# Optimization experiments

Hardware: AMD Instinct MI355X
Metric: run time of the kernel (lower is better)

The kernel has to match this reference:

```python
import jax, jax.numpy as jnp
import numpy as np

BN_EPS = 1e-5


def _gin_layer(x, src, dst, W, b, num_nodes):
    # GINConv with eps=0: h_i = MLP(x_i + sum_{j in N(i)} x_j)
    agg = jax.ops.segment_sum(x[src], dst, num_segments=num_nodes)  # [N, F]
    h = (x + agg) @ W + b
    return jax.nn.relu(h)


def _batchnorm(h, gamma, beta):
    # training-mode BatchNorm1d: biased batch stats over the node dim
    mean = jnp.mean(h, axis=0)
    var = jnp.mean(jnp.square(h - mean), axis=0)
    return (h - mean) * jax.lax.rsqrt(var + BN_EPS) * gamma + beta


def setup_inputs() -> dict:
    key = jax.random.key(0)
    N, E, F, H = 50000, 800000, 128, 128
    ks = jax.random.split(key, 6)
    x = jax.random.normal(ks[0], (N, F), dtype=jnp.float32)
    edge_index = jax.random.randint(ks[1], (2, E), 0, N, dtype=jnp.int64)
    W1 = jax.random.normal(ks[2], (F, H), dtype=jnp.float32) * 0.05
    b1 = jnp.zeros((H,), dtype=jnp.float32)
    W2 = jax.random.normal(ks[3], (H, H), dtype=jnp.float32) * 0.05
    b2 = jnp.zeros((H,), dtype=jnp.float32)
    g1 = jnp.ones((H,), dtype=jnp.float32)
    be1 = jnp.zeros((H,), dtype=jnp.float32)
    g2 = jnp.ones((H,), dtype=jnp.float32)
    be2 = jnp.zeros((H,), dtype=jnp.float32)
    return {"x": x, "edge_index": edge_index, "W1": W1, "b1": b1,
            "W2": W2, "b2": b2, "g1": g1, "be1": be1, "g2": g2, "be2": be2}


def reference(x, edge_index, W1, b1, W2, b2, g1, be1, g2, be2):
    N = x.shape[0]
    src, dst = edge_index[0], edge_index[1]
    h = _gin_layer(x, src, dst, W1, b1, N)
    h = _batchnorm(h, g1, be1)
    h = _gin_layer(h, src, dst, W2, b2, N)
    return _batchnorm(h, g2, be2)
```

## Files before the change

kernel.cpp:

```cpp
#include <hip/hip_runtime.h>
#include <hip/hip_fp16.h>

#define FDIM 128
#define NGRP 8

typedef _Float16 half8_t __attribute__((ext_vector_type(8)));
typedef _Float16 half4_t __attribute__((ext_vector_type(4)));
typedef float float4_t __attribute__((ext_vector_type(4)));


__global__ void zero_kernel(int* __restrict__ p, int n) {
  int i = blockIdx.x * blockDim.x + threadIdx.x;
  if (i < n) p[i] = 0;
}

__global__ void hist_part_kernel(const int* __restrict__ dst, int* __restrict__ deg,
                                 int E, int step) {
  int grp = blockIdx.x & (NGRP - 1);
  int nb = gridDim.x >> 3, bid = blockIdx.x >> 3;
  int lo = grp * step, hi = lo + step;
  int E4 = E >> 2;
  const int4* d4 = (const int4*)dst;
  for (int i = bid * blockDim.x + threadIdx.x; i < E4; i += nb * blockDim.x) {
    int4 d = d4[i];
    if (d.x >= lo && d.x < hi) atomicAdd(&deg[d.x], 1);
    if (d.y >= lo && d.y < hi) atomicAdd(&deg[d.y], 1);
    if (d.z >= lo && d.z < hi) atomicAdd(&deg[d.z], 1);
    if (d.w >= lo && d.w < hi) atomicAdd(&deg[d.w], 1);
  }
  for (int e = (E4 << 2) + bid * blockDim.x + threadIdx.x; e < E; e += nb * blockDim.x) {
    int d = dst[e];
    if (d >= lo && d < hi) atomicAdd(&deg[d], 1);
  }
}

__global__ void scan1_kernel(const int* __restrict__ deg, int* __restrict__ csums, int N) {
  __shared__ int sh[256];
  int t = threadIdx.x, b = blockIdx.x;
  int base = b * 1024;
  int s = 0;
#pragma unroll
  for (int i = 0; i < 4; i++) {
    int idx = base + t + 256 * i;
    if (idx < N) s += deg[idx];
  }
  sh[t] = s; __syncthreads();
  for (int off = 128; off > 0; off >>= 1) {
    if (t < off) sh[t] += sh[t + off];
    __syncthreads();
  }
  if (t == 0) csums[b] = sh[0];
}

__global__ void scan2_kernel(const int* __restrict__ csums, int* __restrict__ coffs, int nchunk) {
  __shared__ int sh[256];
  int t = threadIdx.x;
  int v = (t < nchunk) ? csums[t] : 0;
  sh[t] = v; __syncthreads();
  for (int off = 1; off < 256; off <<= 1) {
    int u = (t >= off) ? sh[t - off] : 0;
    __syncthreads();
    sh[t] += u;
    __syncthreads();
  }
  if (t < nchunk) coffs[t] = sh[t] - v;
}

__global__ void scan3_kernel(const int* __restrict__ deg, const int* __restrict__ coffs,
                             int* __restrict__ row_start, int* __restrict__ fill_pos, int N) {
  __shared__ int sh[256];
  int t = threadIdx.x, b = blockIdx.x;
  int base = b * 1024 + t * 4;
  int d0 = (base + 0 < N) ? deg[base + 0] : 0;
  int d1 = (base + 1 < N) ? deg[base + 1] : 0;
  int d2 = (base + 2 < N) ? deg[base + 2] : 0;
  int d3 = (base + 3 < N) ? deg[base + 3] : 0;
  int l1 = d0, l2 = l1 + d1, l3 = l2 + d2, tot = l3 + d3;
  sh[t] = tot; __syncthreads();
  for (int off = 1; off < 256; off <<= 1) {
    int v = (t >= off) ? sh[t - off] : 0;
    __syncthreads();
    sh[t] += v;
    __syncthreads();
  }
  int excl = sh[t] - tot + coffs[b];
  if (base + 0 < N) { row_start[base + 0] = excl;      fill_pos[base + 0] = excl; }
  if (base + 1 < N) { row_start[base + 1] = excl + l1; fill_pos[base + 1] = excl + l1; }
  if (base + 2 < N) { row_start[base + 2] = excl + l2; fill_pos[base + 2] = excl + l2; }
  if (base + 3 < N) { row_start[base + 3] = excl + l3; fill_pos[base + 3] = excl + l3; }
}

__global__ void place_part_kernel(const int* __restrict__ src, const int* __restrict__ dst,
                                  int* __restrict__ fill_pos, int* __restrict__ ssrc,
                                  int E, int step) {
  int grp = blockIdx.x & (NGRP - 1);
  int nb = gridDim.x >> 3, bid = blockIdx.x >> 3;
  int lo = grp * step, hi = lo + step;
  int E4 = E >> 2;
  const int4* d4 = (const int4*)dst;
  const int4* s4 = (const int4*)src;
  for (int i = bid * blockDim.x + threadIdx.x; i < E4; i += nb * blockDim.x) {
    int4 d = d4[i];
    int4 s = s4[i];
    if (d.x >= lo && d.x < hi) ssrc[atomicAdd(&fill_pos[d.x], 1)] = s.x;
    if (d.y >= lo && d.y < hi) ssrc[atomicAdd(&fill_pos[d.y], 1)] = s.y;
    if (d.z >= lo && d.z < hi) ssrc[atomicAdd(&fill_pos[d.z], 1)] = s.z;
    if (d.w >= lo && d.w < hi) ssrc[atomicAdd(&fill_pos[d.w], 1)] = s.w;
  }
  for (int e = (E4 << 2) + bid * blockDim.x + threadIdx.x; e < E; e += nb * blockDim.x) {
    int d = dst[e];
    if (d >= lo && d < hi) ssrc[atomicAdd(&fill_pos[d], 1)] = src[e];
  }
}


__global__ void cvt_f2h_kernel(const float* __restrict__ in, _Float16* __restrict__ out, int n4) {
  int i = blockIdx.x * blockDim.x + threadIdx.x;
  if (i < n4) {
    float4 v = ((const float4*)in)[i];
    half4_t h;
    h.x = (_Float16)v.x; h.y = (_Float16)v.y; h.z = (_Float16)v.z; h.w = (_Float16)v.w;
    ((half4_t*)out)[i] = h;
  }
}

__global__ void prepw_kernel(const float* __restrict__ W, _Float16* __restrict__ Wf) {
  int tid = blockIdx.x * blockDim.x + threadIdx.x;
  int j = tid & 7, lane = (tid >> 3) & 63, rest = tid >> 9;
  int kb = rest & 3, ct = (rest >> 2) & 1, wave = rest >> 3;
  int quad = lane >> 4, m16 = lane & 15;
  int k = kb * 32 + quad * 8 + j;
  int n = wave * 32 + ct * 16 + m16;
  Wf[tid] = (_Float16)W[k * FDIM + n];
}


__device__ inline float2 up2(unsigned u) {
  __half2 h = *(__half2*)&u;
  return __half22float2(h);
}

template <bool SCALE>
__global__ void agg_kernel(const unsigned* __restrict__ xu, const int* __restrict__ row_start,
                           const int* __restrict__ deg, const int* __restrict__ ssrc,
                           const float* __restrict__ a, unsigned* __restrict__ outu, int N) {
  int wave = (blockIdx.x * blockDim.x + threadIdx.x) >> 6;
  int lane = threadIdx.x & 63;
  if (wave >= N) return;
  float2 c0 = up2(xu[(size_t)wave * 64 + lane]);
  float2 c1 = make_float2(0.f, 0.f), c2 = c1, c3 = c1;
  int start = row_start[wave], d = deg[wave];
  int k = 0;
  for (; k + 7 < d; k += 8) {
    int s0 = ssrc[start + k + 0], s1 = ssrc[start + k + 1];
    int s2 = ssrc[start + k + 2], s3 = ssrc[start + k + 3];
    int s4 = ssrc[start + k + 4], s5 = ssrc[start + k + 5];
    int s6 = ssrc[start + k + 6], s7 = ssrc[start + k + 7];
    unsigned u0 = xu[(size_t)s0 * 64 + lane], u1 = xu[(size_t)s1 * 64 + lane];
    unsigned u2 = xu[(size_t)s2 * 64 + lane], u3 = xu[(size_t)s3 * 64 + lane];
    unsigned u4 = xu[(size_t)s4 * 64 + lane], u5 = xu[(size_t)s5 * 64 + lane];
    unsigned u6 = xu[(size_t)s6 * 64 + lane], u7 = xu[(size_t)s7 * 64 + lane];
    float2 v0 = up2(u0), v1 = up2(u1), v2 = up2(u2), v3 = up2(u3);
    float2 v4 = up2(u4), v5 = up2(u5), v6 = up2(u6), v7 = up2(u7);
    c0.x += v0.x + v4.x; c0.y += v0.y + v4.y;
    c1.x += v1.x + v5.x; c1.y += v1.y + v5.y;
    c2.x += v2.x + v6.x; c2.y += v2.y + v6.y;
    c3.x += v3.x + v7.x; c3.y += v3.y + v7.y;
  }
  for (; k + 1 < d; k += 2) {
    int s0 = ssrc[start + k], s1 = ssrc[start + k + 1];
    unsigned u0 = xu[(size_t)s0 * 64 + lane], u1 = xu[(size_t)s1 * 64 + lane];
    float2 v0 = up2(u0), v1 = up2(u1);
    c0.x += v0.x; c0.y += v0.y;
    c1.x += v1.x; c1.y += v1.y;
  }
  if (k < d) {
    float2 v = up2(xu[(size_t)ssrc[start + k] * 64 + lane]);
    c0.x += v.x; c0.y += v.y;
  }
  float2 acc;
  acc.x = (c0.x + c1.x) + (c2.x + c3.x);
  acc.y = (c0.y + c1.y) + (c2.y + c3.y);
  if (SCALE) {
    float2 av = ((const float2*)a)[lane];
    acc.x *= av.x; acc.y *= av.y;
  }
  __half2 r = __float22half2_rn(acc);
  outu[(size_t)wave * 64 + lane] = *(unsigned*)&r;
}


template <bool LAYER2>
__global__ __launch_bounds__(256) void gemm_kernel(
    const _Float16* __restrict__ in, const _Float16* __restrict__ Wf,
    const float* __restrict__ bias, const float* __restrict__ r2,
    const int* __restrict__ deg, _Float16* __restrict__ outh,
    float* __restrict__ ssum, float* __restrict__ ssq, int N) {
  int t = threadIdx.x;
  int wave = t >> 6, lane = t & 63;
  int quad = lane >> 4, m16 = lane & 15;
  int row0 = blockIdx.x * 64;

  __shared__ float sdn[64];
  if (LAYER2) {
    if (t < 64) {
      int r = row0 + t;
      sdn[t] = (r < N) ? (float)(deg[r] + 1) : 0.f;
    }
    __syncthreads();
  }

  half8_t bf[2][4];
  const half8_t* wf8 = (const half8_t*)Wf;
#pragma unroll
  for (int ct = 0; ct < 2; ct++)
#pragma unroll
    for (int kb = 0; kb < 4; kb++)
      bf[ct][kb] = wf8[(size_t)(((wave * 2 + ct) * 4 + kb) * 64 + lane)];

  float4_t acc[4][2] = {};
#pragma unroll
  for (int rt = 0; rt < 4; rt++) {
    int arow = row0 + rt * 16 + m16;
    int cr = (arow < N) ? arow : N - 1;
#pragma unroll
    for (int kb = 0; kb < 4; kb++) {
      half8_t av = *(const half8_t*)(in + (size_t)cr * FDIM + kb * 32 + quad * 8);
      acc[rt][0] = __builtin_amdgcn_mfma_f32_16x16x32_f16(av, bf[0][kb], acc[rt][0], 0, 0, 0);
      acc[rt][1] = __builtin_amdgcn_mfma_f32_16x16x32_f16(av, bf[1][kb], acc[rt][1], 0, 0, 0);
    }
  }

#pragma unroll
  for (int ct = 0; ct < 2; ct++) {
    int col = wave * 32 + ct * 16 + m16;
    float bv = bias[col];
    float rv = LAYER2 ? r2[col] : 0.f;
    float s = 0.f, q = 0.f;
#pragma unroll
    for (int rt = 0; rt < 4; rt++) {
#pragma unroll
      for (int r = 0; r < 4; r++) {
        int row = row0 + rt * 16 + quad * 4 + r;
        if (row < N) {
          float v = acc[rt][ct][r] + bv;
          if (LAYER2) v += sdn[rt * 16 + quad * 4 + r] * rv;
          v = fmaxf(v, 0.f);
          outh[(size_t)row * FDIM + col] = (_Float16)v;
          s += v; q += v * v;
        }
      }
    }
    s += __shfl_xor(s, 16); q += __shfl_xor(q, 16);
    s += __shfl_xor(s, 32); q += __shfl_xor(q, 32);
    if (quad == 0) {
      atomicAdd(&ssum[col], s);
      atomicAdd(&ssq[col], q);
    }
  }
}


__global__ void coeffs1_kernel(const float* __restrict__ sum, const float* __restrict__ sq,
                               const float* __restrict__ gamma, const float* __restrict__ beta,
                               const float* __restrict__ W2, float* __restrict__ a,
                               float* __restrict__ r2, int N) {
  __shared__ float cc[FDIM];
  int t = threadIdx.x;
  float invn = 1.f / (float)N;
  float mean = sum[t] * invn;
  float var = sq[t] * invn - mean * mean;
  float rs = rsqrtf(var + 1e-5f);
  float av = gamma[t] * rs;
  a[t] = av;
  cc[t] = beta[t] - mean * av;
  __syncthreads();
  float acc = 0.f;
  for (int k = 0; k < FDIM; k++) acc += cc[k] * W2[k * FDIM + t];
  r2[t] = acc;
}

__global__ void coeffs_kernel(const float* __restrict__ sum, const float* __restrict__ sq,
                              const float* __restrict__ gamma, const float* __restrict__ beta,
                              float* __restrict__ a, float* __restrict__ c, int N) {
  int t = threadIdx.x;
  if (t < FDIM) {
    float invn = 1.f / (float)N;
    float mean = sum[t] * invn;
    float var = sq[t] * invn - mean * mean;
    float rs = rsqrtf(var + 1e-5f);
    float av = gamma[t] * rs;
    a[t] = av;
    c[t] = beta[t] - mean * av;
  }
}

__global__ void apply_h_kernel(const uint2* __restrict__ h4, const float* __restrict__ a,
                               const float* __restrict__ c, float4* __restrict__ out, int n4) {
  int i = blockIdx.x * blockDim.x + threadIdx.x;
  if (i < n4) {
    uint2 u = h4[i];
    float2 v0 = up2(u.x), v1 = up2(u.y);
    int c4 = i & 31;
    float4 av = ((const float4*)a)[c4];
    float4 cv = ((const float4*)c)[c4];
    float4 o;
    o.x = av.x * v0.x + cv.x;
    o.y = av.y * v0.y + cv.y;
    o.z = av.z * v1.x + cv.z;
    o.w = av.w * v1.y + cv.w;
    out[i] = o;
  }
}


extern "C" void kernel_launch(void* const* d_in, const int* in_sizes, int n_in,
                              void* d_out, int out_size, void* d_ws, size_t ws_size,
                              hipStream_t stream) {
  const float* x   = (const float*)d_in[0];
  const int*   ei  = (const int*)d_in[1];
  const float* W1  = (const float*)d_in[2];
  const float* b1  = (const float*)d_in[3];
  const float* W2  = (const float*)d_in[4];
  const float* b2  = (const float*)d_in[5];
  const float* g1  = (const float*)d_in[6];
  const float* be1 = (const float*)d_in[7];
  const float* g2  = (const float*)d_in[8];
  const float* be2 = (const float*)d_in[9];
  float* out = (float*)d_out;

  const int N = in_sizes[0] / FDIM;
  const int E = in_sizes[1] / 2;
  const int* src = ei;
  const int* dst = ei + E;

  auto align256 = [](char*& q) { q = (char*)(((uintptr_t)q + 255) & ~(uintptr_t)255); };

  char* p = (char*)d_ws;
  int* deg = (int*)p;        p += (size_t)N * 4;
  float* stats = (float*)p;  p += 1280 * 4;
  align256(p);
  int* row_start = (int*)p;  p += (size_t)N * 4; align256(p);
  int* fill_pos = (int*)p;   p += (size_t)N * 4; align256(p);
  int* csums = (int*)p;      p += 256 * 4;
  int* coffs = (int*)p;      p += 256 * 4; align256(p);
  int* ssrc = (int*)p;       p += (size_t)E * 4; align256(p);
  _Float16* xh  = (_Float16*)p; p += (size_t)N * FDIM * 2; align256(p);
  _Float16* tmp = (_Float16*)p; p += (size_t)N * FDIM * 2; align256(p);
  _Float16* h1  = (_Float16*)p; p += (size_t)N * FDIM * 2; align256(p);
  _Float16* Wf1 = (_Float16*)p; p += FDIM * FDIM * 2;
  _Float16* Wf2 = (_Float16*)p; p += FDIM * FDIM * 2;

  float* s1 = stats + 0,   *q1 = stats + 128;
  float* s2 = stats + 256, *q2 = stats + 384;
  float* a1 = stats + 512, *r2 = stats + 640;
  float* a2 = stats + 768, *c2 = stats + 896;

  const int nchunk = (N + 1023) / 1024;
  const int ntiles = (N + 63) / 64;
  const int step = (N + NGRP - 1) / NGRP;

  int zn = N + 1280;
  zero_kernel<<<(zn + 255) / 256, 256, 0, stream>>>(deg, zn);
  hist_part_kernel<<<NGRP * 128, 256, 0, stream>>>(dst, deg, E, step);
  cvt_f2h_kernel<<<(N * 32 + 255) / 256, 256, 0, stream>>>(x, xh, N * 32);
  prepw_kernel<<<64, 256, 0, stream>>>(W1, Wf1);
  prepw_kernel<<<64, 256, 0, stream>>>(W2, Wf2);
  scan1_kernel<<<nchunk, 256, 0, stream>>>(deg, csums, N);
  scan2_kernel<<<1, 256, 0, stream>>>(csums, coffs, nchunk);
  scan3_kernel<<<nchunk, 256, 0, stream>>>(deg, coffs, row_start, fill_pos, N);
  place_part_kernel<<<NGRP * 128, 256, 0, stream>>>(src, dst, fill_pos, ssrc, E, step);

  agg_kernel<false><<<(N + 3) / 4, 256, 0, stream>>>((const unsigned*)xh, row_start, deg,
                                                     ssrc, nullptr, (unsigned*)tmp, N);
  gemm_kernel<false><<<ntiles, 256, 0, stream>>>(tmp, Wf1, b1, nullptr, nullptr, h1,
                                                 s1, q1, N);
  coeffs1_kernel<<<1, 128, 0, stream>>>(s1, q1, g1, be1, W2, a1, r2, N);

  agg_kernel<true><<<(N + 3) / 4, 256, 0, stream>>>((const unsigned*)h1, row_start, deg,
                                                    ssrc, a1, (unsigned*)tmp, N);
  gemm_kernel<true><<<ntiles, 256, 0, stream>>>(tmp, Wf2, b2, r2, deg, h1, s2, q2, N);
  coeffs_kernel<<<1, 128, 0, stream>>>(s2, q2, g2, be2, a2, c2, N);

  int n4 = N * 32;
  apply_h_kernel<<<(n4 + 255) / 256, 256, 0, stream>>>((const uint2*)h1, a2, c2,
                                                       (float4*)out, n4);
}
```

Measured before the change: 319.9 us.

## Fuse neighbor aggregation into MFMA GEMM via shared-memory tile per layer

```diff
diff --git a/kernel.cpp b/kernel.cpp
--- a/kernel.cpp
+++ b/kernel.cpp
@@ -3,6 +3,7 @@
 
 #define FDIM 128
 #define NGRP 8
+#define LPAD 136
 
 typedef _Float16 half8_t __attribute__((ext_vector_type(8)));
 typedef _Float16 half4_t __attribute__((ext_vector_type(4)));
@@ -101,11 +102,15 @@
   const int4* s4 = (const int4*)src;
   for (int i = bid * blockDim.x + threadIdx.x; i < E4; i += nb * blockDim.x) {
     int4 d = d4[i];
-    int4 s = s4[i];
-    if (d.x >= lo && d.x < hi) ssrc[atomicAdd(&fill_pos[d.x], 1)] = s.x;
-    if (d.y >= lo && d.y < hi) ssrc[atomicAdd(&fill_pos[d.y], 1)] = s.y;
-    if (d.z >= lo && d.z < hi) ssrc[atomicAdd(&fill_pos[d.z], 1)] = s.z;
-    if (d.w >= lo && d.w < hi) ssrc[atomicAdd(&fill_pos[d.w], 1)] = s.w;
+    bool m0 = d.x >= lo && d.x < hi, m1 = d.y >= lo && d.y < hi;
+    bool m2 = d.z >= lo && d.z < hi, m3 = d.w >= lo && d.w < hi;
+    if (m0 | m1 | m2 | m3) {
+      int4 s = s4[i];
+      if (m0) ssrc[atomicAdd(&fill_pos[d.x], 1)] = s.x;
+      if (m1) ssrc[atomicAdd(&fill_pos[d.y], 1)] = s.y;
+      if (m2) ssrc[atomicAdd(&fill_pos[d.z], 1)] = s.z;
+      if (m3) ssrc[atomicAdd(&fill_pos[d.w], 1)] = s.w;
+    }
   }
   for (int e = (E4 << 2) + bid * blockDim.x + threadIdx.x; e < E; e += nb * blockDim.x) {
     int d = dst[e];
@@ -124,8 +129,13 @@
   }
 }
 
-__global__ void prepw_kernel(const float* __restrict__ W, _Float16* __restrict__ Wf) {
-  int tid = blockIdx.x * blockDim.x + threadIdx.x;
+__global__ void prepw2_kernel(const float* __restrict__ W1, _Float16* __restrict__ Wf1,
+                              const float* __restrict__ W2, _Float16* __restrict__ Wf2) {
+  int gid = blockIdx.x * blockDim.x + threadIdx.x;
+  int which = gid >> 14;
+  int tid = gid & 16383;
+  const float* W = which ? W2 : W1;
+  _Float16* Wf = which ? Wf2 : Wf1;
   int j = tid & 7, lane = (tid >> 3) & 63, rest = tid >> 9;
   int kb = rest & 3, ct = (rest >> 2) & 1, wave = rest >> 3;
   int quad = lane >> 4, m16 = lane & 15;
@@ -140,92 +150,88 @@
   return __half22float2(h);
 }
 
-template <bool SCALE>
-__global__ void agg_kernel(const unsigned* __restrict__ xu, const int* __restrict__ row_start,
-                           const int* __restrict__ deg, const int* __restrict__ ssrc,
-                           const float* __restrict__ a, unsigned* __restrict__ outu, int N) {
-  int wave = (blockIdx.x * blockDim.x + threadIdx.x) >> 6;
-  int lane = threadIdx.x & 63;
-  if (wave >= N) return;
-  float2 c0 = up2(xu[(size_t)wave * 64 + lane]);
-  float2 c1 = make_float2(0.f, 0.f), c2 = c1, c3 = c1;
-  int start = row_start[wave], d = deg[wave];
-  int k = 0;
-  for (; k + 7 < d; k += 8) {
-    int s0 = ssrc[start + k + 0], s1 = ssrc[start + k + 1];
-    int s2 = ssrc[start + k + 2], s3 = ssrc[start + k + 3];
-    int s4 = ssrc[start + k + 4], s5 = ssrc[start + k + 5];
-    int s6 = ssrc[start + k + 6], s7 = ssrc[start + k + 7];
-    unsigned u0 = xu[(size_t)s0 * 64 + lane], u1 = xu[(size_t)s1 * 64 + lane];
-    unsigned u2 = xu[(size_t)s2 * 64 + lane], u3 = xu[(size_t)s3 * 64 + lane];
-    unsigned u4 = xu[(size_t)s4 * 64 + lane], u5 = xu[(size_t)s5 * 64 + lane];
-    unsigned u6 = xu[(size_t)s6 * 64 + lane], u7 = xu[(size_t)s7 * 64 + lane];
-    float2 v0 = up2(u0), v1 = up2(u1), v2 = up2(u2), v3 = up2(u3);
-    float2 v4 = up2(u4), v5 = up2(u5), v6 = up2(u6), v7 = up2(u7);
-    c0.x += v0.x + v4.x; c0.y += v0.y + v4.y;
-    c1.x += v1.x + v5.x; c1.y += v1.y + v5.y;
-    c2.x += v2.x + v6.x; c2.y += v2.y + v6.y;
-    c3.x += v3.x + v7.x; c3.y += v3.y + v7.y;
-  }
-  for (; k + 1 < d; k += 2) {
-    int s0 = ssrc[start + k], s1 = ssrc[start + k + 1];
-    unsigned u0 = xu[(size_t)s0 * 64 + lane], u1 = xu[(size_t)s1 * 64 + lane];
-    float2 v0 = up2(u0), v1 = up2(u1);
-    c0.x += v0.x; c0.y += v0.y;
-    c1.x += v1.x; c1.y += v1.y;
-  }
-  if (k < d) {
-    float2 v = up2(xu[(size_t)ssrc[start + k] * 64 + lane]);
-    c0.x += v.x; c0.y += v.y;
-  }
-  float2 acc;
-  acc.x = (c0.x + c1.x) + (c2.x + c3.x);
-  acc.y = (c0.y + c1.y) + (c2.y + c3.y);
-  if (SCALE) {
-    float2 av = ((const float2*)a)[lane];
-    acc.x *= av.x; acc.y *= av.y;
-  }
-  __half2 r = __float22half2_rn(acc);
-  outu[(size_t)wave * 64 + lane] = *(unsigned*)&r;
-}
-
-
 template <bool LAYER2>
-__global__ __launch_bounds__(256) void gemm_kernel(
-    const _Float16* __restrict__ in, const _Float16* __restrict__ Wf,
+__global__ __launch_bounds__(256) void layer_kernel(
+    const unsigned* __restrict__ xu, const int* __restrict__ row_start,
+    const int* __restrict__ deg, const int* __restrict__ ssrc,
+    const float* __restrict__ ascale, const _Float16* __restrict__ Wf,
     const float* __restrict__ bias, const float* __restrict__ r2,
-    const int* __restrict__ deg, _Float16* __restrict__ outh,
-    float* __restrict__ ssum, float* __restrict__ ssq, int N) {
+    _Float16* __restrict__ outh, float* __restrict__ ssum, float* __restrict__ ssq,
+    int N) {
+  __shared__ _Float16 sA[64 * LPAD];
+  __shared__ float sdn[64];
   int t = threadIdx.x;
   int wave = t >> 6, lane = t & 63;
   int quad = lane >> 4, m16 = lane & 15;
   int row0 = blockIdx.x * 64;
 
-  __shared__ float sdn[64];
+  half8_t bf[2][4];
+  const half8_t* wf8 = (const half8_t*)Wf;
+#pragma unroll
+  for (int ct = 0; ct < 2; ct++)
+#pragma unroll
+    for (int kb = 0; kb < 4; kb++)
+      bf[ct][kb] = wf8[(size_t)(((wave * 2 + ct) * 4 + kb) * 64 + lane)];
+
   if (LAYER2) {
     if (t < 64) {
       int r = row0 + t;
       sdn[t] = (r < N) ? (float)(deg[r] + 1) : 0.f;
     }
-    __syncthreads();
-  }
-
-  half8_t bf[2][4];
-  const half8_t* wf8 = (const half8_t*)Wf;
-#pragma unroll
-  for (int ct = 0; ct < 2; ct++)
-#pragma unroll
-    for (int kb = 0; kb < 4; kb++)
-      bf[ct][kb] = wf8[(size_t)(((wave * 2 + ct) * 4 + kb) * 64 + lane)];
+  }
+
+  for (int i = 0; i < 16; i++) {
+    int node = row0 + (wave << 4) + i;
+    if (node >= N) break;
+    float2 c0 = up2(xu[(size_t)node * 64 + lane]);
+    float2 c1 = make_float2(0.f, 0.f), c2 = c1, c3 = c1;
+    int start = row_start[node], d = deg[node];
+    int k = 0;
+    for (; k + 7 < d; k += 8) {
+      int s0 = ssrc[start + k + 0], s1 = ssrc[start + k + 1];
+      int s2 = ssrc[start + k + 2], s3 = ssrc[start + k + 3];
+      int s4 = ssrc[start + k + 4], s5 = ssrc[start + k + 5];
+      int s6 = ssrc[start + k + 6], s7 = ssrc[start + k + 7];
+      unsigned u0 = xu[(size_t)s0 * 64 + lane], u1 = xu[(size_t)s1 * 64 + lane];
+      unsigned u2 = xu[(size_t)s2 * 64 + lane], u3 = xu[(size_t)s3 * 64 + lane];
+      unsigned u4 = xu[(size_t)s4 * 64 + lane], u5 = xu[(size_t)s5 * 64 + lane];
+      unsigned u6 = xu[(size_t)s6 * 64 + lane], u7 = xu[(size_t)s7 * 64 + lane];
+      float2 v0 = up2(u0), v1 = up2(u1), v2 = up2(u2), v3 = up2(u3);
+      float2 v4 = up2(u4), v5 = up2(u5), v6 = up2(u6), v7 = up2(u7);
+      c0.x += v0.x + v4.x; c0.y += v0.y + v4.y;
+      c1.x += v1.x + v5.x; c1.y += v1.y + v5.y;
+      c2.x += v2.x + v6.x; c2.y += v2.y + v6.y;
+      c3.x += v3.x + v7.x; c3.y += v3.y + v7.y;
+    }
+    for (; k + 1 < d; k += 2) {
+      int s0 = ssrc[start + k], s1 = ssrc[start + k + 1];
+      unsigned u0 = xu[(size_t)s0 * 64 + lane], u1 = xu[(size_t)s1 * 64 + lane];
+      float2 v0 = up2(u0), v1 = up2(u1);
+      c0.x += v0.x; c0.y += v0.y;
+      c1.x += v1.x; c1.y += v1.y;
+    }
+    if (k < d) {
+      float2 v = up2(xu[(size_t)ssrc[start + k] * 64 + lane]);
+      c0.x += v.x; c0.y += v.y;
+    }
+    float2 acc;
+    acc.x = (c0.x + c1.x) + (c2.x + c3.x);
+    acc.y = (c0.y + c1.y) + (c2.y + c3.y);
+    if (LAYER2) {
+      float2 av = ((const float2*)ascale)[lane];
+      acc.x *= av.x; acc.y *= av.y;
+    }
+    __half2 r = __float22half2_rn(acc);
+    *(__half2*)&sA[(size_t)((wave << 4) + i) * LPAD + 2 * lane] = r;
+  }
+  __syncthreads();
 
   float4_t acc[4][2] = {};
 #pragma unroll
   for (int rt = 0; rt < 4; rt++) {
-    int arow = row0 + rt * 16 + m16;
-    int cr = (arow < N) ? arow : N - 1;
 #pragma unroll
     for (int kb = 0; kb < 4; kb++) {
-      half8_t av = *(const half8_t*)(in + (size_t)cr * FDIM + kb * 32 + quad * 8);
+      half8_t av = *(const half8_t*)&sA[(size_t)(rt * 16 + m16) * LPAD + kb * 32 + quad * 8];
       acc[rt][0] = __builtin_amdgcn_mfma_f32_16x16x32_f16(av, bf[0][kb], acc[rt][0], 0, 0, 0);
       acc[rt][1] = __builtin_amdgcn_mfma_f32_16x16x32_f16(av, bf[1][kb], acc[rt][1], 0, 0, 0);
     }
@@ -346,8 +352,8 @@
   int* coffs = (int*)p;      p += 256 * 4; align256(p);
   int* ssrc = (int*)p;       p += (size_t)E * 4; align256(p);
   _Float16* xh  = (_Float16*)p; p += (size_t)N * FDIM * 2; align256(p);
-  _Float16* tmp = (_Float16*)p; p += (size_t)N * FDIM * 2; align256(p);
   _Float16* h1  = (_Float16*)p; p += (size_t)N * FDIM * 2; align256(p);
+  _Float16* h2  = (_Float16*)p; p += (size_t)N * FDIM * 2; align256(p);
   _Float16* Wf1 = (_Float16*)p; p += FDIM * FDIM * 2;
   _Float16* Wf2 = (_Float16*)p; p += FDIM * FDIM * 2;
 
@@ -364,25 +370,21 @@
   zero_kernel<<<(zn + 255) / 256, 256, 0, stream>>>(deg, zn);
   hist_part_kernel<<<NGRP * 128, 256, 0, stream>>>(dst, deg, E, step);
   cvt_f2h_kernel<<<(N * 32 + 255) / 256, 256, 0, stream>>>(x, xh, N * 32);
-  prepw_kernel<<<64, 256, 0, stream>>>(W1, Wf1);
-  prepw_kernel<<<64, 256, 0, stream>>>(W2, Wf2);
+  prepw2_kernel<<<128, 256, 0, stream>>>(W1, Wf1, W2, Wf2);
   scan1_kernel<<<nchunk, 256, 0, stream>>>(deg, csums, N);
   scan2_kernel<<<1, 256, 0, stream>>>(csums, coffs, nchunk);
   scan3_kernel<<<nchunk, 256, 0, stream>>>(deg, coffs, row_start, fill_pos, N);
   place_part_kernel<<<NGRP * 128, 256, 0, stream>>>(src, dst, fill_pos, ssrc, E, step);
 
-  agg_kernel<false><<<(N + 3) / 4, 256, 0, stream>>>((const unsigned*)xh, row_start, deg,
-                                                     ssrc, nullptr, (unsigned*)tmp, N);
-  gemm_kernel<false><<<ntiles, 256, 0, stream>>>(tmp, Wf1, b1, nullptr, nullptr, h1,
-                                                 s1, q1, N);
+  layer_kernel<false><<<ntiles, 256, 0, stream>>>((const unsigned*)xh, row_start, deg, ssrc,
+                                                  nullptr, Wf1, b1, nullptr, h1, s1, q1, N);
   coeffs1_kernel<<<1, 128, 0, stream>>>(s1, q1, g1, be1, W2, a1, r2, N);
 
-  agg_kernel<true><<<(N + 3) / 4, 256, 0, stream>>>((const unsigned*)h1, row_start, deg,
-                                                    ssrc, a1, (unsigned*)tmp, N);
-  gemm_kernel<true><<<ntiles, 256, 0, stream>>>(tmp, Wf2, b2, r2, deg, h1, s2, q2, N);
+  layer_kernel<true><<<ntiles, 256, 0, stream>>>((const unsigned*)h1, row_start, deg, ssrc,
+                                                 a1, Wf2, b2, r2, h2, s2, q2, N);
   coeffs_kernel<<<1, 128, 0, stream>>>(s2, q2, g2, be2, a2, c2, N);
 
   int n4 = N * 32;
-  apply_h_kernel<<<(n4 + 255) / 256, 256, 0, stream>>>((const uint2*)h1, a2, c2,
+  apply_h_kernel<<<(n4 + 255) / 256, 256, 0, stream>>>((const uint2*)h2, a2, c2,
                                                        (float4*)out, n4);
 }
```

New measurement: 338.5 us. 1.06x slower.

## Fuse prep, scan and BN-coefficient kernels to cut launch count

Applied to the files above, without the earlier changes.

```diff
diff --git a/kernel.cpp b/kernel.cpp
--- a/kernel.cpp
+++ b/kernel.cpp
@@ -9,10 +9,38 @@
 typedef float float4_t __attribute__((ext_vector_type(4)));
 
 
-__global__ void zero_kernel(int* __restrict__ p, int n) {
-  int i = blockIdx.x * blockDim.x + threadIdx.x;
-  if (i < n) p[i] = 0;
-}
+__global__ void prep_kernel(int* __restrict__ zbase, int zn,
+                            const float* __restrict__ x, _Float16* __restrict__ xh, int n4x,
+                            const float* __restrict__ W1, _Float16* __restrict__ Wf1,
+                            const float* __restrict__ W2, _Float16* __restrict__ Wf2,
+                            int nzb, int ncb) {
+  int b = blockIdx.x, t = threadIdx.x;
+  if (b < nzb) {
+    int i = b * 256 + t;
+    if (i < zn) zbase[i] = 0;
+  } else if (b < nzb + ncb) {
+    int i = (b - nzb) * 256 + t;
+    if (i < n4x) {
+      float4 v = ((const float4*)x)[i];
+      half4_t h;
+      h.x = (_Float16)v.x; h.y = (_Float16)v.y; h.z = (_Float16)v.z; h.w = (_Float16)v.w;
+      ((half4_t*)xh)[i] = h;
+    }
+  } else {
+    int gid = (b - nzb - ncb) * 256 + t;
+    int which = gid >> 14;
+    int tid = gid & 16383;
+    const float* W = which ? W2 : W1;
+    _Float16* Wf = which ? Wf2 : Wf1;
+    int j = tid & 7, lane = (tid >> 3) & 63, rest = tid >> 9;
+    int kb = rest & 3, ct = (rest >> 2) & 1, wave = rest >> 3;
+    int quad = lane >> 4, m16 = lane & 15;
+    int k = kb * 32 + quad * 8 + j;
+    int n = wave * 32 + ct * 16 + m16;
+    Wf[tid] = (_Float16)W[k * FDIM + n];
+  }
+}
+
 
 __global__ void hist_part_kernel(const int* __restrict__ dst, int* __restrict__ deg,
                                  int E, int step) {
@@ -34,41 +62,12 @@
   }
 }
 
-__global__ void scan1_kernel(const int* __restrict__ deg, int* __restrict__ csums, int N) {
+__global__ void scan_fused_kernel(const int* __restrict__ deg,
+                                  unsigned long long* __restrict__ state,
+                                  int* __restrict__ row_start, int* __restrict__ fill_pos,
+                                  int N) {
   __shared__ int sh[256];
-  int t = threadIdx.x, b = blockIdx.x;
-  int base = b * 1024;
-  int s = 0;
-#pragma unroll
-  for (int i = 0; i < 4; i++) {
-    int idx = base + t + 256 * i;
-    if (idx < N) s += deg[idx];
-  }
-  sh[t] = s; __syncthreads();
-  for (int off = 128; off > 0; off >>= 1) {
-    if (t < off) sh[t] += sh[t + off];
-    __syncthreads();
-  }
-  if (t == 0) csums[b] = sh[0];
-}
-
-__global__ void scan2_kernel(const int* __restrict__ csums, int* __restrict__ coffs, int nchunk) {
-  __shared__ int sh[256];
-  int t = threadIdx.x;
-  int v = (t < nchunk) ? csums[t] : 0;
-  sh[t] = v; __syncthreads();
-  for (int off = 1; off < 256; off <<= 1) {
-    int u = (t >= off) ? sh[t - off] : 0;
-    __syncthreads();
-    sh[t] += u;
-    __syncthreads();
-  }
-  if (t < nchunk) coffs[t] = sh[t] - v;
-}
-
-__global__ void scan3_kernel(const int* __restrict__ deg, const int* __restrict__ coffs,
-                             int* __restrict__ row_start, int* __restrict__ fill_pos, int N) {
-  __shared__ int sh[256];
+  __shared__ int s_excl;
   int t = threadIdx.x, b = blockIdx.x;
   int base = b * 1024 + t * 4;
   int d0 = (base + 0 < N) ? deg[base + 0] : 0;
@@ -83,7 +82,28 @@
     sh[t] += v;
     __syncthreads();
   }
-  int excl = sh[t] - tot + coffs[b];
+  if (t == 0) {
+    int block_sum = sh[255];
+    if (b == 0) {
+      atomicExch(&state[0], (2ULL << 32) | (unsigned)block_sum);
+      s_excl = 0;
+    } else {
+      atomicExch(&state[b], (1ULL << 32) | (unsigned)block_sum);
+      int excl = 0;
+      int j = b - 1;
+      for (;;) {
+        unsigned long long v;
+        do { v = atomicAdd(&state[j], 0ULL); } while ((v >> 32) == 0ULL);
+        excl += (int)(unsigned)v;
+        if ((v >> 32) == 2ULL) break;
+        j--;
+      }
+      atomicExch(&state[b], (2ULL << 32) | (unsigned)(excl + block_sum));
+      s_excl = excl;
+    }
+  }
+  __syncthreads();
+  int excl = sh[t] - tot + s_excl;
   if (base + 0 < N) { row_start[base + 0] = excl;      fill_pos[base + 0] = excl; }
   if (base + 1 < N) { row_start[base + 1] = excl + l1; fill_pos[base + 1] = excl + l1; }
   if (base + 2 < N) { row_start[base + 2] = excl + l2; fill_pos[base + 2] = excl + l2; }
@@ -101,37 +121,20 @@
   const int4* s4 = (const int4*)src;
   for (int i = bid * blockDim.x + threadIdx.x; i < E4; i += nb * blockDim.x) {
     int4 d = d4[i];
-    int4 s = s4[i];
-    if (d.x >= lo && d.x < hi) ssrc[atomicAdd(&fill_pos[d.x], 1)] = s.x;
-    if (d.y >= lo && d.y < hi) ssrc[atomicAdd(&fill_pos[d.y], 1)] = s.y;
-    if (d.z >= lo && d.z < hi) ssrc[atomicAdd(&fill_pos[d.z], 1)] = s.z;
-    if (d.w >= lo && d.w < hi) ssrc[atomicAdd(&fill_pos[d.w], 1)] = s.w;
+    bool m0 = d.x >= lo && d.x < hi, m1 = d.y >= lo && d.y < hi;
+    bool m2 = d.z >= lo && d.z < hi, m3 = d.w >= lo && d.w < hi;
+    if (m0 | m1 | m2 | m3) {
+      int4 s = s4[i];
+      if (m0) ssrc[atomicAdd(&fill_pos[d.x], 1)] = s.x;
+      if (m1) ssrc[atomicAdd(&fill_pos[d.y], 1)] = s.y;
+      if (m2) ssrc[atomicAdd(&fill_pos[d.z], 1)] = s.z;
+      if (m3) ssrc[atomicAdd(&fill_pos[d.w], 1)] = s.w;
+    }
   }
   for (int e = (E4 << 2) + bid * blockDim.x + threadIdx.x; e < E; e += nb * blockDim.x) {
     int d = dst[e];
     if (d >= lo && d < hi) ssrc[atomicAdd(&fill_pos[d], 1)] = src[e];
   }
-}
-
-
-__global__ void cvt_f2h_kernel(const float* __restrict__ in, _Float16* __restrict__ out, int n4) {
-  int i = blockIdx.x * blockDim.x + threadIdx.x;
-  if (i < n4) {
-    float4 v = ((const float4*)in)[i];
-    half4_t h;
-    h.x = (_Float16)v.x; h.y = (_Float16)v.y; h.z = (_Float16)v.z; h.w = (_Float16)v.w;
-    ((half4_t*)out)[i] = h;
-  }
-}
-
-__global__ void prepw_kernel(const float* __restrict__ W, _Float16* __restrict__ Wf) {
-  int tid = blockIdx.x * blockDim.x + threadIdx.x;
-  int j = tid & 7, lane = (tid >> 3) & 63, rest = tid >> 9;
-  int kb = rest & 3, ct = (rest >> 2) & 1, wave = rest >> 3;
-  int quad = lane >> 4, m16 = lane & 15;
-  int k = kb * 32 + quad * 8 + j;
-  int n = wave * 32 + ct * 16 + m16;
-  Wf[tid] = (_Float16)W[k * FDIM + n];
 }
 
 
@@ -195,13 +198,18 @@
     const _Float16* __restrict__ in, const _Float16* __restrict__ Wf,
     const float* __restrict__ bias, const float* __restrict__ r2,
     const int* __restrict__ deg, _Float16* __restrict__ outh,
-    float* __restrict__ ssum, float* __restrict__ ssq, int N) {
+    float* __restrict__ ssum, float* __restrict__ ssq,
+    const float* __restrict__ gamma, const float* __restrict__ beta,
+    const float* __restrict__ W2, float* __restrict__ aout, float* __restrict__ cout,
+    int* __restrict__ counter, int N) {
   int t = threadIdx.x;
   int wave = t >> 6, lane = t & 63;
   int quad = lane >> 4, m16 = lane & 15;
   int row0 = blockIdx.x * 64;
 
   __shared__ float sdn[64];
+  __shared__ float scc[FDIM];
+  __shared__ int isLast;
   if (LAYER2) {
     if (t < 64) {
       int r = row0 + t;
@@ -258,42 +266,40 @@
       atomicAdd(&ssq[col], q);
     }
   }
-}
-
-
-__global__ void coeffs1_kernel(const float* __restrict__ sum, const float* __restrict__ sq,
-                               const float* __restrict__ gamma, const float* __restrict__ beta,
-                               const float* __restrict__ W2, float* __restrict__ a,
-                               float* __restrict__ r2, int N) {
-  __shared__ float cc[FDIM];
-  int t = threadIdx.x;
-  float invn = 1.f / (float)N;
-  float mean = sum[t] * invn;
-  float var = sq[t] * invn - mean * mean;
-  float rs = rsqrtf(var + 1e-5f);
-  float av = gamma[t] * rs;
-  a[t] = av;
-  cc[t] = beta[t] - mean * av;
+
   __syncthreads();
-  float acc = 0.f;
-  for (int k = 0; k < FDIM; k++) acc += cc[k] * W2[k * FDIM + t];
-  r2[t] = acc;
-}
-
-__global__ void coeffs_kernel(const float* __restrict__ sum, const float* __restrict__ sq,
-                              const float* __restrict__ gamma, const float* __restrict__ beta,
-                              float* __restrict__ a, float* __restrict__ c, int N) {
-  int t = threadIdx.x;
+  if (t == 0) {
+    __threadfence();
+    int v = atomicAdd(counter, 1);
+    isLast = (v == (int)gridDim.x - 1);
+  }
+  __syncthreads();
+  if (!isLast) return;
+
+  float av = 0.f;
   if (t < FDIM) {
+    float sm = atomicAdd(&ssum[t], 0.f);
+    float qv = atomicAdd(&ssq[t], 0.f);
     float invn = 1.f / (float)N;
-    float mean = sum[t] * invn;
-    float var = sq[t] * invn - mean * mean;
+    float mean = sm * invn;
+    float var = qv * invn - mean * mean;
     float rs = rsqrtf(var + 1e-5f);
-    float av = gamma[t] * rs;
-    a[t] = av;
-    c[t] = beta[t] - mean * av;
-  }
-}
+    av = gamma[t] * rs;
+    aout[t] = av;
+    float cv = beta[t] - mean * av;
+    if (LAYER2) cout[t] = cv;
+    else scc[t] = cv;
+  }
+  if (!LAYER2) {
+    __syncthreads();
+    if (t < FDIM) {
+      float acc2 = 0.f;
+      for (int k = 0; k < FDIM; k++) acc2 += scc[k] * W2[k * FDIM + t];
+      cout[t] = acc2;
+    }
+  }
+}
+
 
 __global__ void apply_h_kernel(const uint2* __restrict__ h4, const float* __restrict__ a,
                                const float* __restrict__ c, float4* __restrict__ out, int n4) {
@@ -337,17 +343,16 @@
   auto align256 = [](char*& q) { q = (char*)(((uintptr_t)q + 255) & ~(uintptr_t)255); };
 
   char* p = (char*)d_ws;
-  int* deg = (int*)p;        p += (size_t)N * 4;
-  float* stats = (float*)p;  p += 1280 * 4;
+  int* deg = (int*)p;                    p += (size_t)N * 4;
+  float* stats = (float*)p;              p += 1280 * 4;
+  unsigned long long* state = (unsigned long long*)p; p += 64 * 8;
   align256(p);
   int* row_start = (int*)p;  p += (size_t)N * 4; align256(p);
   int* fill_pos = (int*)p;   p += (size_t)N * 4; align256(p);
-  int* csums = (int*)p;      p += 256 * 4;
-  int* coffs = (int*)p;      p += 256 * 4; align256(p);
   int* ssrc = (int*)p;       p += (size_t)E * 4; align256(p);
   _Float16* xh  = (_Float16*)p; p += (size_t)N * FDIM * 2; align256(p);
-  _Float16* tmp = (_Float16*)p; p += (size_t)N * FDIM * 2; align256(p);
   _Float16* h1  = (_Float16*)p; p += (size_t)N * FDIM * 2; align256(p);
+  _Float16* h2  = (_Float16*)p; p += (size_t)N * FDIM * 2; align256(p);
   _Float16* Wf1 = (_Float16*)p; p += FDIM * FDIM * 2;
   _Float16* Wf2 = (_Float16*)p; p += FDIM * FDIM * 2;
 
@@ -355,34 +360,35 @@
   float* s2 = stats + 256, *q2 = stats + 384;
   float* a1 = stats + 512, *r2 = stats + 640;
   float* a2 = stats + 768, *c2 = stats + 896;
+  int* cnt1 = (int*)(stats + 1024);
+  int* cnt2 = (int*)(stats + 1025);
 
   const int nchunk = (N + 1023) / 1024;
   const int ntiles = (N + 63) / 64;
   const int step = (N + NGRP - 1) / NGRP;
 
-  int zn = N + 1280;
-  zero_kernel<<<(zn + 255) / 256, 256, 0, stream>>>(deg, zn);
+  const int zn = N + 1280 + 128;
+  const int nzb = (zn + 255) / 256;
+  const int n4x = N * 32;
+  const int ncb = (n4x + 255) / 256;
+
+  prep_kernel<<<nzb + ncb + 128, 256, 0, stream>>>((int*)deg, zn, x, xh, n4x,
+                                                   W1, Wf1, W2, Wf2, nzb, ncb);
   hist_part_kernel<<<NGRP * 128, 256, 0, stream>>>(dst, deg, E, step);
-  cvt_f2h_kernel<<<(N * 32 + 255) / 256, 256, 0, stream>>>(x, xh, N * 32);
-  prepw_kernel<<<64, 256, 0, stream>>>(W1, Wf1);
-  prepw_kernel<<<64, 256, 0, stream>>>(W2, Wf2);
-  scan1_kernel<<<nchunk, 256, 0, stream>>>(deg, csums, N);
-  scan2_kernel<<<1, 256, 0, stream>>>(csums, coffs, nchunk);
-  scan3_kernel<<<nchunk, 256, 0, stream>>>(deg, coffs, row_start, fill_pos, N);
+  scan_fused_kernel<<<nchunk, 256, 0, stream>>>(deg, state, row_start, fill_pos, N);
   place_part_kernel<<<NGRP * 128, 256, 0, stream>>>(src, dst, fill_pos, ssrc, E, step);
 
   agg_kernel<false><<<(N + 3) / 4, 256, 0, stream>>>((const unsigned*)xh, row_start, deg,
-                                                     ssrc, nullptr, (unsigned*)tmp, N);
-  gemm_kernel<false><<<ntiles, 256, 0, stream>>>(tmp, Wf1, b1, nullptr, nullptr, h1,
-                                                 s1, q1, N);
-  coeffs1_kernel<<<1, 128, 0, stream>>>(s1, q1, g1, be1, W2, a1, r2, N);
+                                                     ssrc, nullptr, (unsigned*)h2, N);
+  gemm_kernel<false><<<ntiles, 256, 0, stream>>>(h2, Wf1, b1, nullptr, nullptr, h1,
+                                                 s1, q1, g1, be1, W2, a1, r2, cnt1, N);
 
   agg_kernel<true><<<(N + 3) / 4, 256, 0, stream>>>((const unsigned*)h1, row_start, deg,
-                                                    ssrc, a1, (unsigned*)tmp, N);
-  gemm_kernel<true><<<ntiles, 256, 0, stream>>>(tmp, Wf2, b2, r2, deg, h1, s2, q2, N);
-  coeffs_kernel<<<1, 128, 0, stream>>>(s2, q2, g2, be2, a2, c2, N);
+                                                    ssrc, a1, (unsigned*)xh, N);
+  gemm_kernel<true><<<ntiles, 256, 0, stream>>>(xh, Wf2, b2, r2, deg, h2,
+                                                s2, q2, g2, be2, nullptr, a2, c2, cnt2, N);
 
   int n4 = N * 32;
-  apply_h_kernel<<<(n4 + 255) / 256, 256, 0, stream>>>((const uint2*)h1, a2, c2,
+  apply_h_kernel<<<(n4 + 255) / 256, 256, 0, stream>>>((const uint2*)h2, a2, c2,
                                                        (float4*)out, n4);
 }
```

New measurement: 341.7 us. +6.8%, slower.
